# Kernel optimization log

Measured on AMD Instinct MI355X. Metric: run time of the kernel, lower is better.

Reference implementation:

```python
import jax, jax.numpy as jnp
import numpy as np

N_HEAD = 4
GROUPS = 32
EPS = 1e-5


def _group_norm(x, w, b):
    B, C, H, W = x.shape
    g = x.reshape(B, GROUPS, C // GROUPS, H, W)
    mu = g.mean(axis=(2, 3, 4), keepdims=True)
    var = ((g - mu) ** 2).mean(axis=(2, 3, 4), keepdims=True)
    g = (g - mu) * jax.lax.rsqrt(var + EPS)
    return g.reshape(B, C, H, W) * w[None, :, None, None] + b[None, :, None, None]


def _l2norm(x):
    # F.normalize(x, dim=-1): x / max(||x||_2, 1e-12)
    n = jnp.sqrt(jnp.sum(x * x, axis=-1, keepdims=True))
    return x / jnp.maximum(n, 1e-12)


def _masked_softmax(attn, kk):
    # topk indices -> scatter 1s -> masked softmax (faithful to torch scatter_ path)
    idx = jax.lax.top_k(attn, kk)[1]                      # [B,H,c,kk]
    mask = jax.nn.one_hot(idx, attn.shape[-1], dtype=attn.dtype).sum(-2)  # [B,H,c,c]
    return jax.nn.softmax(jnp.where(mask > 0, attn, -jnp.inf), axis=-1)


def setup_inputs() -> dict:
    key = jax.random.key(0)
    ks = jax.random.split(key, 8)
    B, C, H, W = 4, 256, 128, 128
    x = jax.random.normal(ks[0], (B, C, H, W), jnp.float32)
    gn_w = 1.0 + 0.02 * jax.random.normal(ks[1], (C,), jnp.float32)
    gn_b = 0.02 * jax.random.normal(ks[2], (C,), jnp.float32)
    w_qkv = jax.random.normal(ks[3], (3 * C, C), jnp.float32) / np.sqrt(C).astype(np.float32)
    w_dw = jax.random.normal(ks[4], (3 * C, 1, 3, 3), jnp.float32) / 3.0
    w_out = jax.random.normal(ks[5], (C, C), jnp.float32) / np.sqrt(C).astype(np.float32)
    b_out = 0.01 * jax.random.normal(ks[6], (C,), jnp.float32)
    temperature = jnp.ones((N_HEAD, 1, 1), jnp.float32)
    attn_w = jnp.full((4,), 0.2, jnp.float32)  # attn1..attn4 combine weights
    return dict(x=x, gn_w=gn_w, gn_b=gn_b, w_qkv=w_qkv, w_dw=w_dw,
                w_out=w_out, b_out=b_out, temperature=temperature, attn_w=attn_w)


def reference(x, gn_w, gn_b, w_qkv, w_dw, w_out, b_out, temperature, attn_w):
    B, C, H, W = x.shape
    c = C // N_HEAD
    xn = _group_norm(x, gn_w, gn_b)
    # 1x1 conv (no bias)
    qkv = jnp.einsum('oi,bihw->bohw', w_qkv, xn)
    # 3x3 depthwise conv, padding=1, groups=3C, no bias
    qkv = jax.lax.conv_general_dilated(
        qkv, w_dw, window_strides=(1, 1), padding=((1, 1), (1, 1)),
        feature_group_count=3 * C,
        dimension_numbers=('NCHW', 'OIHW', 'NCHW'))
    q, k, v = jnp.split(qkv, 3, axis=1)
    # b (head c) h w -> b head c (h w)
    q = q.reshape(B, N_HEAD, c, H * W)
    k = k.reshape(B, N_HEAD, c, H * W)
    v = v.reshape(B, N_HEAD, c, H * W)
    q = _l2norm(q)
    k = _l2norm(k)
    # FFT cross-correlation attention (fftshift over ALL axes, as torch default)
    q_fft = jnp.fft.fftshift(jnp.fft.rfft2(q))   # [B,H,c,HW//2+1] complex
    k_fft = jnp.fft.fftshift(jnp.fft.rfft2(k))
    attn = jnp.einsum('bhcf,bhdf->bhcd', q_fft, k_fft) * temperature  # complex [B,H,c,c]
    attn = jnp.fft.irfft2(jnp.fft.ifftshift(attn), s=(c, c))          # real [B,H,c,c]
    ks_list = [c // 2, (c * 2) // 3, (c * 3) // 4, (c * 4) // 5]
    out = None
    for i, kk in enumerate(ks_list):
        a = _masked_softmax(attn, kk)
        o = jnp.einsum('bhcd,bhds->bhcs', a, v) * attn_w[i]
        out = o if out is None else out + o
    out = out.reshape(B, C, H, W)
    out = jnp.einsum('oi,bihw->bohw', w_out, out) + b_out[None, :, None, None]
    return out
```

## Files before the change

### kernel.cpp

```cpp
#include <hip/hip_runtime.h>
#include <math.h>

#define NC 256
#define CH3 768
#define HWSZ 16384

typedef __attribute__((ext_vector_type(8))) short short8;
typedef __attribute__((ext_vector_type(4))) float f32x4;
typedef __attribute__((ext_vector_type(4))) unsigned int u32x4;

static const size_t OFF_TW1   = 0;
static const size_t OFF_TW2   = 32768;
static const size_t OFF_HM    = 65536;
static const size_t OFF_SCALE = 65600;
static const size_t OFF_SHIFT = 66624;
static const size_t OFF_PACK  = 67648;
static const size_t OFF_AW    = 182336;
static const size_t OFF_GNP   = 444480;
static const size_t SHARED_END= 446528;

static const size_t R_QKV  = 0;
static const size_t R_SCR  = 12582912;
static const size_t R_H    = 25165824;
static const size_t R_PP   = 29360128;
static const size_t R_RP   = 30408704;
static const size_t R_ATTN = 31457280;
static const size_t R_ACOMB= 31473664;
static const size_t R_PS   = 31490048;
static const size_t R_RS   = 31506432;
static const size_t R_DWP  = 31522816;
static const size_t R_SSUM = 31532032;
static const size_t R_SALT = 31532800;
static const size_t R_SSQ  = 31533568;
static const size_t RSTRIDE= 31534336;
static const size_t HNOFF  = 8388608;

#define TDA_RH 0
#define TDA_RL 8192
#define TDA_IH 16384
#define TDA_IL 24576
#define ETA_RH 32768
#define ETA_RL 40960
#define ETA_IH 49152
#define ETA_IL 57344
#define STB_RH 65536
#define STB_RL 73728
#define STB_IH 81920
#define STB_IL 90112
#define STB_NIH 98304
#define STB_NIL 106496

#define AWQ_H 0
#define AWQ_L 98304
#define AWO_H 196608
#define AWO_L 229376

__device__ inline unsigned short b16rn(float x){
  unsigned u = __float_as_uint(x);
  return (unsigned short)((u + 0x7FFFu + ((u>>16)&1u)) >> 16);
}
__device__ inline unsigned int pk_hi(float x, float y){
  return (__float_as_uint(x)>>16) | (__float_as_uint(y) & 0xFFFF0000u);
}
__device__ inline unsigned int pk_lo(float x, float y){
  float xl = x - __uint_as_float(__float_as_uint(x) & 0xFFFF0000u);
  float yl = y - __uint_as_float(__float_as_uint(y) & 0xFFFF0000u);
  return (unsigned)b16rn(xl) | ((unsigned)b16rn(yl)<<16);
}
__device__ inline short8 ld8g(const unsigned int* p){ return *(const short8*)p; }

__global__ __launch_bounds__(256) void init_tables_k(float* __restrict__ ws){
  int idx = blockIdx.x*256 + threadIdx.x;
  float2* tw1 = (float2*)(ws + OFF_TW1);
  float2* tw2 = (float2*)(ws + OFF_TW2);
  unsigned int* pk = (unsigned int*)(ws + OFF_PACK);
  const double P2 = 6.283185307179586476925286766559005;
  int m = idx >> 7, k = idx & 127;
  double a2 = P2 * (double)(m*k) / 16384.0;
  tw1[idx] = make_float2((float)cos(a2), (float)(-sin(a2)));
  tw2[idx] = make_float2((float)cos(a2), (float)( sin(a2)));
  if (idx < 64){
    double acc = 0.0;
    for (int v = 1; v < 32; v++) acc += sin(P2 * (double)((v*idx) & 63) / 64.0);
    ws[OFF_HM + idx] = (float)(-acc / 32.0);
  }
  if (idx < 8192){
    int r = idx >> 6, kp = idx & 63;
    int k0 = 2*kp, k1 = 2*kp+1;
    double a0 = P2 * (double)((r*k0) & 127) / 128.0;
    double a1 = P2 * (double)((r*k1) & 127) / 128.0;
    float c0 = (float)cos(a0), c1 = (float)cos(a1);
    float s0 = (float)sin(a0), s1 = (float)sin(a1);
    pk[TDA_RH + idx] = pk_hi(c0, c1);  pk[TDA_RL + idx] = pk_lo(c0, c1);
    pk[TDA_IH + idx] = pk_hi(-s0,-s1); pk[TDA_IL + idx] = pk_lo(-s0,-s1);
    pk[ETA_RH + idx] = pk_hi(c0, c1);  pk[ETA_RL + idx] = pk_lo(c0, c1);
    pk[ETA_IH + idx] = pk_hi(s0, s1);  pk[ETA_IL + idx] = pk_lo(s0, s1);
    float sr0, si0, sr1, si1;
    {
      int d0 = (r - k0) & 127, d1 = (r - k1) & 127;
      if (d0 == 0){ sr0 = 64.f; si0 = 0.f; }
      else if ((d0 & 1) == 0){ sr0 = 0.f; si0 = 0.f; }
      else { double th = 3.1415926535897932384626 * (double)d0 / 128.0;
             sr0 = 1.f; si0 = (float)(cos(th)/sin(th)); }
      if (d1 == 0){ sr1 = 64.f; si1 = 0.f; }
      else if ((d1 & 1) == 0){ sr1 = 0.f; si1 = 0.f; }
      else { double th = 3.1415926535897932384626 * (double)d1 / 128.0;
             sr1 = 1.f; si1 = (float)(cos(th)/sin(th)); }
    }
    pk[STB_RH + idx]  = pk_hi(sr0, sr1);  pk[STB_RL + idx]  = pk_lo(sr0, sr1);
    pk[STB_IH + idx]  = pk_hi(si0, si1);  pk[STB_IL + idx]  = pk_lo(si0, si1);
    pk[STB_NIH + idx] = pk_hi(-si0,-si1); pk[STB_NIL + idx] = pk_lo(-si0,-si1);
  }
}

__global__ __launch_bounds__(256) void wpack_k(const float* __restrict__ wqkv, const float* __restrict__ wout,
                                               unsigned int* __restrict__ aw){
  int id = blockIdx.x*256 + threadIdx.x;
  int row = id >> 7, kp = id & 127;
  if (row < CH3){
    float v0 = wqkv[row*256 + 2*kp], v1 = wqkv[row*256 + 2*kp + 1];
    aw[AWQ_H + row*128 + kp] = pk_hi(v0, v1);
    aw[AWQ_L + row*128 + kp] = pk_lo(v0, v1);
  } else {
    int r2 = row - CH3;
    float v0 = wout[r2*256 + 2*kp], v1 = wout[r2*256 + 2*kp + 1];
    aw[AWO_H + r2*128 + kp] = pk_hi(v0, v1);
    aw[AWO_L + r2*128 + kp] = pk_lo(v0, v1);
  }
}

__global__ __launch_bounds__(256) void gn_part_k(const float* __restrict__ x, float2* __restrict__ part){
  int id = blockIdx.x;
  const float4* p = (const float4*)(x + (size_t)id*HWSZ);
  int tid = threadIdx.x;
  float s = 0.f, sq = 0.f;
  #pragma unroll
  for (int i = 0; i < 16; i++){
    float4 v = p[tid + i*256];
    s  += v.x+v.y+v.z+v.w;
    sq += v.x*v.x+v.y*v.y+v.z*v.z+v.w*v.w;
  }
  __shared__ float r1[256], r2[256];
  r1[tid]=s; r2[tid]=sq; __syncthreads();
  for (int off=128; off; off>>=1){
    if (tid<off){ r1[tid]+=r1[tid+off]; r2[tid]+=r2[tid+off]; }
    __syncthreads();
  }
  if (tid==0) part[id] = make_float2(r1[0], r2[0]);
}
__global__ __launch_bounds__(128) void gn_fin_k(const float2* __restrict__ part, const float* __restrict__ gw,
                                                const float* __restrict__ gb, float* __restrict__ scale,
                                                float* __restrict__ shift){
  int bg = threadIdx.x;
  int b = bg >> 5, g = bg & 31;
  float s = 0.f, sq = 0.f;
  #pragma unroll
  for (int i = 0; i < 8; i++){
    float2 v = part[b*NC + g*8 + i];
    s += v.x; sq += v.y;
  }
  const float n = 8.0f*HWSZ;
  float mu = s/n, var = sq/n - mu*mu;
  float rs = rsqrtf(var + 1e-5f);
  for (int i = 0; i < 8; i++){
    int ch = g*8 + i;
    float sc = rs * gw[ch];
    scale[b*NC + ch] = sc;
    shift[b*NC + ch] = gb[ch] - mu*sc;
  }
}

__global__ __launch_bounds__(256) void packx_k(const float* __restrict__ xbase, const float* __restrict__ scale,
                                               const float* __restrict__ shift, float* __restrict__ R0,
                                               size_t rstride){
  int bz = blockIdx.z;
  const float* xb = xbase + (size_t)bz*NC*HWSZ;
  const float* sc = scale + bz*NC;
  const float* sh = shift + bz*NC;
  unsigned int* BqH = (unsigned int*)(R0 + (size_t)bz*rstride + R_H);
  unsigned int* BqL = BqH + 2097152;
  int kb = blockIdx.y;
  int n = blockIdx.x*256 + threadIdx.x;
  float v[8];
  #pragma unroll
  for (int c = 0; c < 8; c++){
    int ch = kb*8 + c;
    v[c] = xb[(size_t)ch*HWSZ + n]*sc[ch] + sh[ch];
  }
  u32x4 h, l;
  #pragma unroll
  for (int q = 0; q < 4; q++){
    h[q] = pk_hi(v[2*q], v[2*q+1]);
    l[q] = pk_lo(v[2*q], v[2*q+1]);
  }
  *(u32x4*)&BqH[((size_t)kb*HWSZ + n)*4] = h;
  *(u32x4*)&BqL[((size_t)kb*HWSZ + n)*4] = l;
}

__global__ __launch_bounds__(256) void gemm_pk(const unsigned int* __restrict__ Ah, const unsigned int* __restrict__ Al,
                                               const unsigned int* __restrict__ Bh0, const unsigned int* __restrict__ Bl0,
                                               const float* __restrict__ bias, float* __restrict__ C0,
                                               size_t bstride, size_t cstride){
  const unsigned int* Bh = Bh0 + (size_t)blockIdx.z*bstride;
  const unsigned int* Bl = Bl0 + (size_t)blockIdx.z*bstride;
  float* C = C0 + (size_t)blockIdx.z*cstride;
  int tid = threadIdx.x;
  int lane = tid & 63, wid = tid >> 6;
  int m0 = blockIdx.y*128, n0 = blockIdx.x*128;
  int wr = (wid>>1)*64, wc = (wid&1)*64;
  int lr = lane & 15, lk = lane >> 4;
  f32x4 acc[4][4] = {};
  size_t aoff[4], boff[4];
  #pragma unroll
  for (int i=0;i<4;i++) aoff[i] = (size_t)(m0 + wr + i*16 + lr)*128 + lk*4;
  #pragma unroll
  for (int j=0;j<4;j++) boff[j] = ((size_t)lk*HWSZ + n0 + wc + j*16 + lr)*4;
  short8 aH[2][4], aL[2][4], bH[2][4], bL[2][4];
  #pragma unroll
  for (int i=0;i<4;i++){ aH[0][i] = ld8g(Ah + aoff[i]); aL[0][i] = ld8g(Al + aoff[i]); }
  #pragma unroll
  for (int j=0;j<4;j++){ bH[0][j] = ld8g(Bh + boff[j]); bL[0][j] = ld8g(Bl + boff[j]); }
  #pragma unroll
  for (int kt = 0; kt < 8; kt++){
    int cur = kt & 1, nxt = cur ^ 1;
    if (kt < 7){
      size_t da = (size_t)(kt+1)*16;
      size_t db = (size_t)(kt+1)*4*HWSZ*4;
      #pragma unroll
      for (int i=0;i<4;i++){ aH[nxt][i] = ld8g(Ah + aoff[i] + da); aL[nxt][i] = ld8g(Al + aoff[i] + da); }
      #pragma unroll
      for (int j=0;j<4;j++){ bH[nxt][j] = ld8g(Bh + boff[j] + db); bL[nxt][j] = ld8g(Bl + boff[j] + db); }
    }
    #pragma unroll
    for (int i=0;i<4;i++)
      #pragma unroll
      for (int j=0;j<4;j++){
        acc[i][j] = __builtin_amdgcn_mfma_f32_16x16x32_bf16(aH[cur][i], bH[cur][j], acc[i][j], 0,0,0);
        acc[i][j] = __builtin_amdgcn_mfma_f32_16x16x32_bf16(aH[cur][i], bL[cur][j], acc[i][j], 0,0,0);
        acc[i][j] = __builtin_amdgcn_mfma_f32_16x16x32_bf16(aL[cur][i], bH[cur][j], acc[i][j], 0,0,0);
      }
  }
  #pragma unroll
  for (int i=0;i<4;i++){
    #pragma unroll
    for (int e=0;e<4;e++){
      int row = m0 + wr + i*16 + lk*4 + e;
      float bb = bias ? bias[row] : 0.0f;
      #pragma unroll
      for (int j=0;j<4;j++)
        C[(size_t)row*HWSZ + n0 + wc + j*16 + lr] = acc[i][j][e] + bb;
    }
  }
}

__global__ __launch_bounds__(256) void dwconv_tiled_k(float* __restrict__ R0, size_t rstride,
                                                      const float* __restrict__ wdw){
  float* Rb = R0 + (size_t)blockIdx.y*rstride;
  int blk = blockIdx.x;
  int ch = blk >> 2, sl = blk & 3;
  int h0 = sl*32;
  const float* in = Rb + R_SCR + (size_t)ch*HWSZ;
  float* part = Rb + R_DWP;
  float w[9];
  #pragma unroll
  for (int i=0;i<9;i++) w[i] = wdw[ch*9+i];
  __shared__ float tile[34][132];
  __shared__ float r0[256], r1[256], r2[256];
  int tid = threadIdx.x;
  #pragma unroll
  for (int i = 0; i < 5; i++){
    int id = tid + i*256;
    if (id < 1088){
      int r = id >> 5, c4 = id & 31;
      int gh = h0 - 1 + r;
      float4 v = (gh >= 0 && gh < 128) ? *(const float4*)&in[gh*128 + c4*4]
                                       : make_float4(0.f,0.f,0.f,0.f);
      *(float4*)&tile[r][c4*4] = v;
    }
  }
  __syncthreads();
  float s=0.f, sa=0.f, sq=0.f;
  #pragma unroll
  for (int it=0; it<4; it++){
    int idx = it*256 + tid;
    int lh = idx >> 5;
    int xq = idx & 31;
    int xb4 = xq*4;
    float o[4];
    #pragma unroll
    for (int e=0;e<4;e++){
      int xw = xb4 + e;
      float acc = 0.f;
      #pragma unroll
      for (int ky=0; ky<3; ky++){
        const float* tr = &tile[lh+ky][xw];
        if (xw > 0)   acc += tr[-1]*w[ky*3+0];
                      acc += tr[ 0]*w[ky*3+1];
        if (xw < 127) acc += tr[ 1]*w[ky*3+2];
      }
      o[e] = acc;
      s += acc; sq += acc*acc;
      sa += (e & 1) ? -acc : acc;
    }
    int sbase = (h0+lh)*128 + xb4;
    if (ch < 256){
      unsigned short* QHo = (unsigned short*)(Rb + R_QKV);
      unsigned short* QLo = (unsigned short*)(Rb + R_QKV + 2097152);
      size_t ro = (size_t)ch*HWSZ;
      #pragma unroll
      for (int e=0;e<4;e++){
        int sf = (16384 - (sbase+e)) & 16383;
        unsigned u = __float_as_uint(o[e]);
        QHo[ro + sf] = (unsigned short)(u >> 16);
        QLo[ro + sf] = b16rn(o[e] - __uint_as_float(u & 0xFFFF0000u));
      }
    } else if (ch < 512){
      *(float4*)&(Rb + R_QKV + (size_t)ch*HWSZ)[sbase] = make_float4(o[0],o[1],o[2],o[3]);
      unsigned short* KHo = (unsigned short*)(Rb + R_H);
      unsigned short* KLo = (unsigned short*)(Rb + R_H + 2097152);
      size_t ro = (size_t)(ch-256)*HWSZ;
      #pragma unroll
      for (int e=0;e<4;e++){
        unsigned u = __float_as_uint(o[e]);
        KHo[ro + sbase+e] = (unsigned short)(u >> 16);
        KLo[ro + sbase+e] = b16rn(o[e] - __uint_as_float(u & 0xFFFF0000u));
      }
    } else {
      *(float4*)&(Rb + R_QKV + (size_t)ch*HWSZ)[sbase] = make_float4(o[0],o[1],o[2],o[3]);
    }
  }
  r0[tid]=s; r1[tid]=sa; r2[tid]=sq; __syncthreads();
  for (int off=128; off; off>>=1){
    if (tid<off){ r0[tid]+=r0[tid+off]; r1[tid]+=r1[tid+off]; r2[tid]+=r2[tid+off]; }
    __syncthreads();
  }
  if (tid==0){ part[blk]=r0[0]; part[3072+blk]=r1[0]; part[6144+blk]=r2[0]; }
}

__global__ __launch_bounds__(256) void fft1_mfma_k(const float* __restrict__ ws, float* __restrict__ R0,
                                                   size_t rstride){
  float* Rb = R0 + (size_t)blockIdx.y*rstride;
  const float* Kb = Rb + R_QKV + (size_t)256*HWSZ;
  float2* Tc = (float2*)(Rb + R_SCR);
  const unsigned int* PK = (const unsigned int*)(ws + OFF_PACK);
  const float2* tw1 = (const float2*)(ws + OFF_TW1);
  __shared__ unsigned int Bth[128][20], Btl[128][20];
  int tid = threadIdx.x;
  int lane = tid & 63, wid = tid >> 6;
  int wr = (wid>>1)*64, wc = (wid&1)*64;
  int lr = lane & 15, lk = lane >> 4;
  int row = blockIdx.x;
  const float* src = Kb + (size_t)row*HWSZ;
  f32x4 aR[4][4] = {}, aI[4][4] = {};
  int bc = tid & 127, grp = tid >> 7;
  for (int kt = 0; kt < 4; kt++){
    #pragma unroll
    for (int p=0;p<8;p++){
      int kp = grp*8 + p;
      int a = kt*32 + 2*kp;
      float v0 = src[a*128 + bc], v1 = src[(a+1)*128 + bc];
      Bth[bc][kp] = pk_hi(v0, v1);
      Btl[bc][kp] = pk_lo(v0, v1);
    }
    __syncthreads();
    short8 bh[4], bl[4];
    #pragma unroll
    for (int j=0;j<4;j++){
      bh[j] = *(const short8*)&Bth[wc + j*16 + lr][lk*4];
      bl[j] = *(const short8*)&Btl[wc + j*16 + lr][lk*4];
    }
    #pragma unroll
    for (int i=0;i<4;i++){
      int off = (wr + i*16 + lr)*64 + kt*16 + lk*4;
      short8 ahR = ld8g(PK + TDA_RH + off), alR = ld8g(PK + TDA_RL + off);
      short8 ahI = ld8g(PK + TDA_IH + off), alI = ld8g(PK + TDA_IL + off);
      #pragma unroll
      for (int j=0;j<4;j++){
        aR[i][j] = __builtin_amdgcn_mfma_f32_16x16x32_bf16(ahR, bh[j], aR[i][j], 0,0,0);
        aR[i][j] = __builtin_amdgcn_mfma_f32_16x16x32_bf16(ahR, bl[j], aR[i][j], 0,0,0);
        aR[i][j] = __builtin_amdgcn_mfma_f32_16x16x32_bf16(alR, bh[j], aR[i][j], 0,0,0);
        aI[i][j] = __builtin_amdgcn_mfma_f32_16x16x32_bf16(ahI, bh[j], aI[i][j], 0,0,0);
        aI[i][j] = __builtin_amdgcn_mfma_f32_16x16x32_bf16(ahI, bl[j], aI[i][j], 0,0,0);
        aI[i][j] = __builtin_amdgcn_mfma_f32_16x16x32_bf16(alI, bh[j], aI[i][j], 0,0,0);
      }
    }
    __syncthreads();
  }
  #pragma unroll
  for (int i=0;i<4;i++)
    #pragma unroll
    for (int e=0;e<4;e++){
      int m = wr + i*16 + lk*4 + e;
      #pragma unroll
      for (int j=0;j<4;j++){
        int col = wc + j*16 + lr;
        float2 t = tw1[m*128 + col];
        float r = aR[i][j][e], im = aI[i][j][e];
        Tc[(size_t)m*32768 + row*128 + col] = make_float2(r*t.x - im*t.y, r*t.y + im*t.x);
      }
    }
}

__global__ __launch_bounds__(256) void fft2_mfma_k(const float* __restrict__ ws, float* __restrict__ R0,
                                                   size_t rstride){
  float* Rb = R0 + (size_t)blockIdx.y*rstride;
  float2* TU = (float2*)(Rb + R_SCR);
  const unsigned int* PK = (const unsigned int*)(ws + OFF_PACK);
  const float2* tw2 = (const float2*)(ws + OFF_TW2);
  __shared__ unsigned int ARh[128][20], ARl[128][20], AIh[128][20], AIl[128][20];
  int tid = threadIdx.x;
  int lane = tid & 63, wid = tid >> 6;
  int wr = (wid>>1)*64, wc = (wid&1)*64;
  int lr = lane & 15, lk = lane >> 4;
  int m0 = blockIdx.x*128;
  f32x4 aR[4][4] = {}, aI[4][4] = {};
  const float* Tf = (const float*)TU;
  for (int kt = 0; kt < 4; kt++){
    #pragma unroll
    for (int s=0;s<8;s++){
      int id = tid + s*256;
      int r = id >> 4, kp = id & 15;
      int k = kt*32 + 2*kp;
      float4 v = *(const float4*)&Tf[((size_t)(m0+r)*128 + k)*2];
      ARh[r][kp] = pk_hi(v.x, v.z); ARl[r][kp] = pk_lo(v.x, v.z);
      AIh[r][kp] = pk_hi(v.y, v.w); AIl[r][kp] = pk_lo(v.y, v.w);
    }
    __syncthreads();
    short8 ahR[4], alR[4], ahI[4], alI[4];
    #pragma unroll
    for (int i=0;i<4;i++){
      int ar = wr + i*16 + lr;
      ahR[i] = *(const short8*)&ARh[ar][lk*4];
      alR[i] = *(const short8*)&ARl[ar][lk*4];
      ahI[i] = *(const short8*)&AIh[ar][lk*4];
      alI[i] = *(const short8*)&AIl[ar][lk*4];
    }
    #pragma unroll
    for (int j=0;j<4;j++){
      int boff = (wc + j*16 + lr)*64 + kt*16 + lk*4;
      short8 bhR = ld8g(PK + STB_RH + boff), blR = ld8g(PK + STB_RL + boff);
      short8 bhI = ld8g(PK + STB_IH + boff), blI = ld8g(PK + STB_IL + boff);
      short8 bhN = ld8g(PK + STB_NIH + boff), blN = ld8g(PK + STB_NIL + boff);
      #pragma unroll
      for (int i=0;i<4;i++){
        aR[i][j] = __builtin_amdgcn_mfma_f32_16x16x32_bf16(ahR[i], bhR, aR[i][j], 0,0,0);
        aR[i][j] = __builtin_amdgcn_mfma_f32_16x16x32_bf16(ahR[i], blR, aR[i][j], 0,0,0);
        aR[i][j] = __builtin_amdgcn_mfma_f32_16x16x32_bf16(alR[i], bhR, aR[i][j], 0,0,0);
        aR[i][j] = __builtin_amdgcn_mfma_f32_16x16x32_bf16(ahI[i], bhN, aR[i][j], 0,0,0);
        aR[i][j] = __builtin_amdgcn_mfma_f32_16x16x32_bf16(ahI[i], blN, aR[i][j], 0,0,0);
        aR[i][j] = __builtin_amdgcn_mfma_f32_16x16x32_bf16(alI[i], bhN, aR[i][j], 0,0,0);
        aI[i][j] = __builtin_amdgcn_mfma_f32_16x16x32_bf16(ahR[i], bhI, aI[i][j], 0,0,0);
        aI[i][j] = __builtin_amdgcn_mfma_f32_16x16x32_bf16(ahR[i], blI, aI[i][j], 0,0,0);
        aI[i][j] = __builtin_amdgcn_mfma_f32_16x16x32_bf16(alR[i], bhI, aI[i][j], 0,0,0);
        aI[i][j] = __builtin_amdgcn_mfma_f32_16x16x32_bf16(ahI[i], bhR, aI[i][j], 0,0,0);
        aI[i][j] = __builtin_amdgcn_mfma_f32_16x16x32_bf16(ahI[i], blR, aI[i][j], 0,0,0);
        aI[i][j] = __builtin_amdgcn_mfma_f32_16x16x32_bf16(alI[i], bhR, aI[i][j], 0,0,0);
      }
    }
    __syncthreads();
  }
  #pragma unroll
  for (int i=0;i<4;i++)
    #pragma unroll
    for (int e=0;e<4;e++){
      int m = m0 + wr + i*16 + lk*4 + e;
      int f0 = m >> 8;
      #pragma unroll
      for (int j=0;j<4;j++){
        int col = wc + j*16 + lr;
        float2 t = tw2[f0*128 + col];
        float r = aR[i][j][e], im = aI[i][j][e];
        TU[(size_t)m*128 + col] = make_float2(r*t.x - im*t.y, r*t.y + im*t.x);
      }
    }
}

__global__ __launch_bounds__(256) void fft3_mfma_k(const float* __restrict__ ws, float* __restrict__ R0,
                                                   size_t rstride){
  float* Rb = R0 + (size_t)blockIdx.y*rstride;
  const float2* U = (const float2*)(Rb + R_SCR);
  unsigned short* HHo = (unsigned short*)(Rb + R_SCR + HNOFF);
  unsigned short* HLo = (unsigned short*)(Rb + R_SCR + HNOFF + 2097152);
  const unsigned int* PK = (const unsigned int*)(ws + OFF_PACK);
  __shared__ unsigned int BRh[128][20], BRl[128][20], BIh[128][20], BIl[128][20];
  int tid = threadIdx.x;
  int lane = tid & 63, wid = tid >> 6;
  int wr = (wid>>1)*64, wc = (wid&1)*64;
  int lr = lane & 15, lk = lane >> 4;
  int brow = blockIdx.x;
  f32x4 ac[4][4] = {};
  int bc = tid & 127, grp = tid >> 7;
  for (int kt = 0; kt < 4; kt++){
    #pragma unroll
    for (int p=0;p<8;p++){
      int kp = grp*8 + p;
      int k = kt*32 + 2*kp;
      float2 v0 = U[((size_t)k*256 + brow)*128 + bc];
      float2 v1 = U[((size_t)(k+1)*256 + brow)*128 + bc];
      BRh[bc][kp] = pk_hi(v0.x, v1.x); BRl[bc][kp] = pk_lo(v0.x, v1.x);
      BIh[bc][kp] = pk_hi(v0.y, v1.y); BIl[bc][kp] = pk_lo(v0.y, v1.y);
    }
    __syncthreads();
    short8 ahR[4], alR[4], ahI[4], alI[4];
    #pragma unroll
    for (int i=0;i<4;i++){
      int off = (wr + i*16 + lr)*64 + kt*16 + lk*4;
      ahR[i] = ld8g(PK + ETA_RH + off); alR[i] = ld8g(PK + ETA_RL + off);
      ahI[i] = ld8g(PK + ETA_IH + off); alI[i] = ld8g(PK + ETA_IL + off);
    }
    #pragma unroll
    for (int j=0;j<4;j++){
      int col = wc + j*16 + lr;
      short8 bhR = *(const short8*)&BRh[col][lk*4];
      short8 blR = *(const short8*)&BRl[col][lk*4];
      short8 bhI = *(const short8*)&BIh[col][lk*4];
      short8 blI = *(const short8*)&BIl[col][lk*4];
      #pragma unroll
      for (int i=0;i<4;i++){
        ac[i][j] = __builtin_amdgcn_mfma_f32_16x16x32_bf16(ahR[i], bhI, ac[i][j], 0,0,0);
        ac[i][j] = __builtin_amdgcn_mfma_f32_16x16x32_bf16(ahR[i], blI, ac[i][j], 0,0,0);
        ac[i][j] = __builtin_amdgcn_mfma_f32_16x16x32_bf16(alR[i], bhI, ac[i][j], 0,0,0);
        ac[i][j] = __builtin_amdgcn_mfma_f32_16x16x32_bf16(ahI[i], bhR, ac[i][j], 0,0,0);
        ac[i][j] = __builtin_amdgcn_mfma_f32_16x16x32_bf16(ahI[i], blR, ac[i][j], 0,0,0);
        ac[i][j] = __builtin_amdgcn_mfma_f32_16x16x32_bf16(alI[i], bhR, ac[i][j], 0,0,0);
      }
    }
    __syncthreads();
  }
  #pragma unroll
  for (int i=0;i<4;i++)
    #pragma unroll
    for (int e=0;e<4;e++){
      int m = wr + i*16 + lk*4 + e;
      #pragma unroll
      for (int j=0;j<4;j++){
        int col = wc + j*16 + lr;
        float v = ac[i][j][e];
        unsigned u = __float_as_uint(v);
        size_t o = (size_t)brow*HWSZ + m*128 + col;
        HHo[o] = (unsigned short)(u >> 16);
        HLo[o] = b16rn(v - __uint_as_float(u & 0xFFFF0000u));
      }
    }
}

__global__ __launch_bounds__(256) void pri3_k(float* __restrict__ R0, size_t rstride){
  float* Rb = R0 + (size_t)blockIdx.z*rstride;
  int sp = blockIdx.x, head = blockIdx.y;
  const unsigned short* QH = (const unsigned short*)(Rb + R_QKV);
  const unsigned short* QL = (const unsigned short*)(Rb + R_QKV + 2097152);
  const unsigned short* KH = (const unsigned short*)(Rb + R_H);
  const unsigned short* KL = (const unsigned short*)(Rb + R_H + 2097152);
  const unsigned short* HH = (const unsigned short*)(Rb + R_SCR + HNOFF);
  const unsigned short* HL = (const unsigned short*)(Rb + R_SCR + HNOFF + 2097152);
  float* Pp = Rb + R_PP;
  float* Rp = Rb + R_RP;
  int tid = threadIdx.x, lane = tid & 63, wid = tid >> 6;
  int wr = (wid>>1)*32, wc = (wid&1)*32;
  int lr = lane & 15, lk = lane >> 4;
  size_t qoff[2], koff[2];
  #pragma unroll
  for (int i=0;i<2;i++) qoff[i] = (size_t)(head*64 + wr + i*16 + lr)*HWSZ + sp*256 + lk*8;
  #pragma unroll
  for (int j=0;j<2;j++) koff[j] = (size_t)(head*64 + wc + j*16 + lr)*HWSZ + sp*256 + lk*8;
  f32x4 aP[2][2] = {}, aRi[2][2] = {};
  short8 qh[2][2], ql[2][2], k1h[2][2], k1l[2][2], k2h[2][2], k2l[2][2];
#define LDPRI(B,T) { int d = (T)*32; \
    _Pragma("unroll") \
    for (int i=0;i<2;i++){ \
      qh[B][i] = *(const short8*)(QH + qoff[i] + d); \
      ql[B][i] = *(const short8*)(QL + qoff[i] + d); } \
    _Pragma("unroll") \
    for (int j=0;j<2;j++){ \
      k1h[B][j] = *(const short8*)(KH + koff[j] + d); \
      k1l[B][j] = *(const short8*)(KL + koff[j] + d); \
      k2h[B][j] = *(const short8*)(HH + koff[j] + d); \
      k2l[B][j] = *(const short8*)(HL + koff[j] + d); } }
  LDPRI(0,0);
  #pragma unroll
  for (int kt = 0; kt < 8; kt++){
    int cur = kt & 1;
    if (kt < 7) LDPRI(cur^1, kt+1);
    #pragma unroll
    for (int i=0;i<2;i++)
      #pragma unroll
      for (int j=0;j<2;j++){
        aP[i][j]  = __builtin_amdgcn_mfma_f32_16x16x32_bf16(qh[cur][i], k1h[cur][j], aP[i][j], 0,0,0);
        aP[i][j]  = __builtin_amdgcn_mfma_f32_16x16x32_bf16(qh[cur][i], k1l[cur][j], aP[i][j], 0,0,0);
        aP[i][j]  = __builtin_amdgcn_mfma_f32_16x16x32_bf16(ql[cur][i], k1h[cur][j], aP[i][j], 0,0,0);
        aRi[i][j] = __builtin_amdgcn_mfma_f32_16x16x32_bf16(qh[cur][i], k2h[cur][j], aRi[i][j], 0,0,0);
        aRi[i][j] = __builtin_amdgcn_mfma_f32_16x16x32_bf16(qh[cur][i], k2l[cur][j], aRi[i][j], 0,0,0);
        aRi[i][j] = __builtin_amdgcn_mfma_f32_16x16x32_bf16(ql[cur][i], k2h[cur][j], aRi[i][j], 0,0,0);
      }
  }
#undef LDPRI
  size_t obase = ((size_t)(sp*4 + head)) << 12;
  #pragma unroll
  for (int i=0;i<2;i++)
    #pragma unroll
    for (int e=0;e<4;e++){
      int row = wr + i*16 + lk*4 + e;
      #pragma unroll
      for (int j=0;j<2;j++){
        int col = wc + j*16 + lr;
        size_t o = obase + (size_t)row*64 + col;
        Pp[o] = aP[i][j][e];
        Rp[o] = aRi[i][j][e];
      }
    }
}

__global__ __launch_bounds__(256) void red_k(float* __restrict__ R0, size_t rstride){
  float* Rb = R0 + (size_t)blockIdx.y*rstride;
  const float* Pp = Rb + R_PP;
  const float* Rp = Rb + R_RP;
  float* Ps = Rb + R_PS;
  float* Rs = Rb + R_RS;
  int tid = threadIdx.x;
  #pragma unroll
  for (int rep=0; rep<2; rep++){
    int g = blockIdx.x*512 + rep*256 + tid;
    int head = g >> 12, loc = g & 4095;
    float p = 0.f, ri = 0.f;
    for (int sp=0; sp<64; sp++){
      size_t o = ((size_t)(sp*4+head)<<12) + loc;
      p += Pp[o]; ri += Rp[o];
    }
    Ps[g] = p; Rs[g] = ri;
  }
  if (blockIdx.x == 0){
    const float* part = Rb + R_DWP;
    for (int ch = tid; ch < CH3; ch += 256){
      float s=0.f, sa=0.f, sq=0.f;
      #pragma unroll
      for (int sl=0; sl<4; sl++){
        s  += part[ch*4+sl];
        sa += part[3072+ch*4+sl];
        sq += part[6144+ch*4+sl];
      }
      Rb[R_SSUM+ch]=s; Rb[R_SALT+ch]=sa; Rb[R_SSQ+ch]=sq;
    }
  }
}

__global__ __launch_bounds__(256) void attn_build_k(const float* __restrict__ ws, float* __restrict__ R0,
                                                    size_t rstride, const float* __restrict__ temperature){
  float* Rb = R0 + (size_t)blockIdx.y*rstride;
  const float* Ps   = Rb + R_PS;
  const float* Rs   = Rb + R_RS;
  const float* ssum = Rb + R_SSUM;
  const float* salt = Rb + R_SALT;
  const float* ssq  = Rb + R_SSQ;
  float* attn = Rb + R_ATTN;
  const float* hmg  = ws + OFF_HM;
  __shared__ float Rn[64][65], Ril[64][65], hm[64];
  int head = blockIdx.x;
  int tid = threadIdx.x;
  if (tid < 64) hm[tid] = hmg[tid];
  for (int t=0;t<16;t++){
    int idx = tid + t*256; int c = idx>>6, d = idx&63;
    float P = Ps[head*4096 + idx], Ri = Rs[head*4096 + idx];
    int qch = head*64 + c;
    int kch = 256 + head*64 + d;
    float qs=ssum[qch], qa=salt[qch], qn=fmaxf(sqrtf(ssq[qch]), 1e-12f);
    float ks=ssum[kch], ka=salt[kch], kn=fmaxf(sqrtf(ssq[kch]), 1e-12f);
    float Rr = 0.5f*(16384.0f*P + qs*ks + qa*ka);
    float sc = 1.0f/(qn*kn);
    Rn[c][d]  = Rr*sc;
    Ril[c][d] = Ri*sc;
  }
  __syncthreads();
  float tmp2 = temperature[(head+2)&3];
  for (int t=0;t<16;t++){
    int idx = tid + t*256; int c = idx>>6, e = idx&63;
    float s = Rn[c][e];
    #pragma unroll 8
    for (int d=0; d<64; d++) s += Ril[c][d]*hm[(e-d)&63];
    attn[((size_t)head<<12) + (size_t)(c*64+e)] = s*tmp2;
  }
}

__global__ __launch_bounds__(64) void topk_k(float* __restrict__ R0, size_t rstride,
                                             const float* __restrict__ attn_w){
  float* Rb = R0 + (size_t)blockIdx.y*rstride;
  const float* attn = Rb + R_ATTN;
  float* Acomb = Rb + R_ACOMB;
  int blk = blockIdx.x;
  int tid = threadIdx.x;
  __shared__ float row[64];
  float v = attn[(size_t)blk*64 + tid];
  row[tid] = v;
  __syncthreads();
  int rank = 0; float vmax = -1e30f;
  for (int l=0;l<64;l++){
    float w = row[l];
    if (w > v || (w == v && l < tid)) rank++;
    vmax = fmaxf(vmax, w);
  }
  float e = expf(v - vmax);
  const int kks[4] = {32,42,48,51};
  float denom[4];
  #pragma unroll
  for (int i=0;i<4;i++){
    float x = (rank < kks[i]) ? e : 0.0f;
    #pragma unroll
    for (int off=32; off; off>>=1) x += __shfl_xor(x, off);
    denom[i] = x;
  }
  float wgt = 0.f;
  #pragma unroll
  for (int i=0;i<4;i++) if (rank < kks[i]) wgt += attn_w[i] / denom[i];
  Acomb[(size_t)blk*64 + tid] = e * wgt;
}

__global__ __launch_bounds__(256) void av_k(float* __restrict__ R0, size_t rstride){
  float* Rb = R0 + (size_t)blockIdx.z*rstride;
  const float* Acomb = Rb + R_ACOMB;
  unsigned int* BqH = (unsigned int*)(Rb + R_H);
  unsigned int* BqL = BqH + 2097152;
  int head = blockIdx.y;
  int n0 = blockIdx.x*64;
  const float* Vb = Rb + R_QKV + (size_t)(512 + head*64)*HWSZ;
  __shared__ float As[64][65], Bs[16][65];
  int tid=threadIdx.x, tx=tid&15, ty=tid>>4;
  for (int t=0;t<16;t++){ int idx=tid+t*256; As[idx>>6][idx&63] = Acomb[((size_t)head<<12)+idx]; }
  __syncthreads();
  float acc[4][4]={};
  for (int k0=0;k0<64;k0+=16){
    #pragma unroll
    for (int i=0;i<4;i++){ int id=tid+i*256; int nn=id&63, k=id>>6;
      Bs[k][nn] = Vb[(size_t)(k0+k)*HWSZ + n0+nn]; }
    __syncthreads();
    #pragma unroll
    for (int k=0;k<16;k++){
      float a[4], bv[4];
      #pragma unroll
      for (int i=0;i<4;i++) a[i]=As[ty*4+i][k0+k];
      #pragma unroll
      for (int j=0;j<4;j++) bv[j]=Bs[k][tx*4+j];
      #pragma unroll
      for (int i=0;i<4;i++)
        #pragma unroll
        for (int j=0;j<4;j++) acc[i][j] += a[i]*bv[j];
    }
    __syncthreads();
  }
  int kpa = head*32 + ty*2;
  int kba = kpa >> 2, qa = kpa & 3;
  int kpb = kpa + 1;
  int kbb = kpb >> 2, qb = kpb & 3;
  #pragma unroll
  for (int j=0;j<4;j++){
    int n = n0 + tx*4 + j;
    BqH[((size_t)kba*HWSZ + n)*4 + qa] = pk_hi(acc[0][j], acc[1][j]);
    BqL[((size_t)kba*HWSZ + n)*4 + qa] = pk_lo(acc[0][j], acc[1][j]);
    BqH[((size_t)kbb*HWSZ + n)*4 + qb] = pk_hi(acc[2][j], acc[3][j]);
    BqL[((size_t)kbb*HWSZ + n)*4 + qb] = pk_lo(acc[2][j], acc[3][j]);
  }
}

extern "C" void kernel_launch(void* const* d_in, const int* in_sizes, int n_in,
                              void* d_out, int out_size, void* d_ws, size_t ws_size,
                              hipStream_t stream) {
  const float* x     = (const float*)d_in[0];
  const float* gn_w  = (const float*)d_in[1];
  const float* gn_b  = (const float*)d_in[2];
  const float* w_qkv = (const float*)d_in[3];
  const float* w_dw  = (const float*)d_in[4];
  const float* w_out = (const float*)d_in[5];
  const float* b_out = (const float*)d_in[6];
  const float* temperature = (const float*)d_in[7];
  const float* attn_w = (const float*)d_in[8];
  float* out = (float*)d_out;
  float* ws  = (float*)d_ws;
  unsigned int* AW = (unsigned int*)(ws + OFF_AW);
  float* R0 = ws + SHARED_END;
  const size_t CHW = (size_t)NC*HWSZ;

  size_t need2 = (SHARED_END + 2*RSTRIDE)*sizeof(float);
  size_t need4 = (SHARED_END + 4*RSTRIDE)*sizeof(float);
  int zb = (ws_size >= need4) ? 4 : (ws_size >= need2) ? 2 : 1;

  init_tables_k<<<64,256,0,stream>>>(ws);
  wpack_k<<<512,256,0,stream>>>(w_qkv, w_out, AW);
  gn_part_k<<<1024,256,0,stream>>>(x, (float2*)(ws+OFF_GNP));
  gn_fin_k<<<1,128,0,stream>>>((const float2*)(ws+OFF_GNP), gn_w, gn_b,
                               ws+OFF_SCALE, ws+OFF_SHIFT);

  for (int b0 = 0; b0 < 4; b0 += zb){
    packx_k<<<dim3(64,32,zb),256,0,stream>>>(x + (size_t)b0*CHW, ws+OFF_SCALE+b0*NC,
                                             ws+OFF_SHIFT+b0*NC, R0, RSTRIDE);
    gemm_pk<<<dim3(128,6,zb),256,0,stream>>>(AW+AWQ_H, AW+AWQ_L,
                                             (unsigned int*)(R0+R_H), (unsigned int*)(R0+R_H)+2097152,
                                             nullptr, R0+R_SCR, RSTRIDE, RSTRIDE);
    dwconv_tiled_k<<<dim3(3072,zb),256,0,stream>>>(R0, RSTRIDE, w_dw);
    fft1_mfma_k<<<dim3(256,zb),256,0,stream>>>(ws, R0, RSTRIDE);
    fft2_mfma_k<<<dim3(256,zb),256,0,stream>>>(ws, R0, RSTRIDE);
    fft3_mfma_k<<<dim3(256,zb),256,0,stream>>>(ws, R0, RSTRIDE);
    pri3_k<<<dim3(64,4,zb),256,0,stream>>>(R0, RSTRIDE);
    red_k<<<dim3(32,zb),256,0,stream>>>(R0, RSTRIDE);
    attn_build_k<<<dim3(4,zb),256,0,stream>>>(ws, R0, RSTRIDE, temperature);
    topk_k<<<dim3(256,zb),64,0,stream>>>(R0, RSTRIDE, attn_w);
    av_k<<<dim3(256,4,zb),256,0,stream>>>(R0, RSTRIDE);
    gemm_pk<<<dim3(128,2,zb),256,0,stream>>>(AW+AWO_H, AW+AWO_L,
                                             (unsigned int*)(R0+R_H), (unsigned int*)(R0+R_H)+2097152,
                                             b_out, out + (size_t)b0*CHW, RSTRIDE, CHW);
  }
}
```

Baseline: 825.1 us.

## Store FFT intermediates as pre-split bf16 hi/lo planes, drop LDS staging

The FFT stage kernels now write intermediates as separate bf16 high/low planes in layouts the next stage can load directly as MFMA fragments, instead of fp32 complex buffers that were re-split through shared memory. fft1 reads the K planes already produced by dwconv, so the fp32 K copy is no longer stored. fft2 and fft3 drop their LDS staging and barriers, and fft2 is split into 512 smaller blocks. This cuts conversion work and intermediate memory traffic, but the direct global fragment loads and the new strided layouts may coalesce less well.

Result: slower. 906.5 us (+9.9%).

```diff
diff --git a/kernel.cpp b/kernel.cpp
--- a/kernel.cpp
+++ b/kernel.cpp
@@ -33,7 +33,8 @@
 static const size_t R_SALT = 31532800;
 static const size_t R_SSQ  = 31533568;
 static const size_t RSTRIDE= 31534336;
-static const size_t HNOFF  = 8388608;
+static const size_t UROFF  = 4194304;
+static const size_t UIOFF  = 8388608;
 
 #define TDA_RH 0
 #define TDA_RL 8192
@@ -68,6 +69,12 @@
   return (unsigned)b16rn(xl) | ((unsigned)b16rn(yl)<<16);
 }
 __device__ inline short8 ld8g(const unsigned int* p){ return *(const short8*)p; }
+__device__ inline short8 ld8s(const unsigned short* p){ return *(const short8*)p; }
+__device__ inline void wr_split(unsigned short* H, unsigned short* L, size_t o, float v){
+  unsigned u = __float_as_uint(v);
+  H[o] = (unsigned short)(u >> 16);
+  L[o] = b16rn(v - __uint_as_float(u & 0xFFFF0000u));
+}
 
 __global__ __launch_bounds__(256) void init_tables_k(float* __restrict__ ws){
   int idx = blockIdx.x*256 + threadIdx.x;
@@ -310,21 +317,15 @@
       #pragma unroll
       for (int e=0;e<4;e++){
         int sf = (16384 - (sbase+e)) & 16383;
-        unsigned u = __float_as_uint(o[e]);
-        QHo[ro + sf] = (unsigned short)(u >> 16);
-        QLo[ro + sf] = b16rn(o[e] - __uint_as_float(u & 0xFFFF0000u));
+        wr_split(QHo, QLo, ro + sf, o[e]);
       }
     } else if (ch < 512){
-      *(float4*)&(Rb + R_QKV + (size_t)ch*HWSZ)[sbase] = make_float4(o[0],o[1],o[2],o[3]);
       unsigned short* KHo = (unsigned short*)(Rb + R_H);
       unsigned short* KLo = (unsigned short*)(Rb + R_H + 2097152);
       size_t ro = (size_t)(ch-256)*HWSZ;
       #pragma unroll
-      for (int e=0;e<4;e++){
-        unsigned u = __float_as_uint(o[e]);
-        KHo[ro + sbase+e] = (unsigned short)(u >> 16);
-        KLo[ro + sbase+e] = b16rn(o[e] - __uint_as_float(u & 0xFFFF0000u));
-      }
+      for (int e=0;e<4;e++)
+        wr_split(KHo, KLo, ro + sbase+e, o[e]);
     } else {
       *(float4*)&(Rb + R_QKV + (size_t)ch*HWSZ)[sbase] = make_float4(o[0],o[1],o[2],o[3]);
     }
@@ -340,8 +341,12 @@
 __global__ __launch_bounds__(256) void fft1_mfma_k(const float* __restrict__ ws, float* __restrict__ R0,
                                                    size_t rstride){
   float* Rb = R0 + (size_t)blockIdx.y*rstride;
-  const float* Kb = Rb + R_QKV + (size_t)256*HWSZ;
-  float2* Tc = (float2*)(Rb + R_SCR);
+  const unsigned short* KH = (const unsigned short*)(Rb + R_H);
+  const unsigned short* KL = (const unsigned short*)(Rb + R_H + 2097152);
+  unsigned short* TRH = (unsigned short*)(Rb + R_SCR);
+  unsigned short* TRL = TRH + 4194304;
+  unsigned short* TIH = TRL + 4194304;
+  unsigned short* TIL = TIH + 4194304;
   const unsigned int* PK = (const unsigned int*)(ws + OFF_PACK);
   const float2* tw1 = (const float2*)(ws + OFF_TW1);
   __shared__ unsigned int Bth[128][20], Btl[128][20];
@@ -350,7 +355,6 @@
   int wr = (wid>>1)*64, wc = (wid&1)*64;
   int lr = lane & 15, lk = lane >> 4;
   int row = blockIdx.x;
-  const float* src = Kb + (size_t)row*HWSZ;
   f32x4 aR[4][4] = {}, aI[4][4] = {};
   int bc = tid & 127, grp = tid >> 7;
   for (int kt = 0; kt < 4; kt++){
@@ -358,9 +362,9 @@
     for (int p=0;p<8;p++){
       int kp = grp*8 + p;
       int a = kt*32 + 2*kp;
-      float v0 = src[a*128 + bc], v1 = src[(a+1)*128 + bc];
-      Bth[bc][kp] = pk_hi(v0, v1);
-      Btl[bc][kp] = pk_lo(v0, v1);
+      size_t o0 = (size_t)row*HWSZ + a*128 + bc;
+      Bth[bc][kp] = (unsigned)KH[o0] | ((unsigned)KH[o0+128] << 16);
+      Btl[bc][kp] = (unsigned)KL[o0] | ((unsigned)KL[o0+128] << 16);
     }
     __syncthreads();
     short8 bh[4], bl[4];
@@ -396,7 +400,10 @@
         int col = wc + j*16 + lr;
         float2 t = tw1[m*128 + col];
         float r = aR[i][j][e], im = aI[i][j][e];
-        Tc[(size_t)m*32768 + row*128 + col] = make_float2(r*t.x - im*t.y, r*t.y + im*t.x);
+        float vr = r*t.x - im*t.y, vi = r*t.y + im*t.x;
+        size_t o = (size_t)m*32768 + row*128 + col;
+        wr_split(TRH, TRL, o, vr);
+        wr_split(TIH, TIL, o, vi);
       }
     }
 }
@@ -404,36 +411,32 @@
 __global__ __launch_bounds__(256) void fft2_mfma_k(const float* __restrict__ ws, float* __restrict__ R0,
                                                    size_t rstride){
   float* Rb = R0 + (size_t)blockIdx.y*rstride;
-  float2* TU = (float2*)(Rb + R_SCR);
+  const unsigned short* TRH = (const unsigned short*)(Rb + R_SCR);
+  const unsigned short* TRL = TRH + 4194304;
+  const unsigned short* TIH = TRL + 4194304;
+  const unsigned short* TIL = TIH + 4194304;
+  unsigned short* URH = (unsigned short*)(Rb + R_QKV + UROFF);
+  unsigned short* URL = URH + 4194304;
+  unsigned short* UIH = (unsigned short*)(Rb + R_SCR + UIOFF);
+  unsigned short* UIL = UIH + 4194304;
   const unsigned int* PK = (const unsigned int*)(ws + OFF_PACK);
   const float2* tw2 = (const float2*)(ws + OFF_TW2);
-  __shared__ unsigned int ARh[128][20], ARl[128][20], AIh[128][20], AIl[128][20];
-  int tid = threadIdx.x;
-  int lane = tid & 63, wid = tid >> 6;
-  int wr = (wid>>1)*64, wc = (wid&1)*64;
+  int tid = threadIdx.x, lane = tid & 63, wid = tid >> 6;
+  int row = blockIdx.x >> 1, mh = blockIdx.x & 1;
+  int wr = (wid>>1)*32, wc = (wid&1)*64;
   int lr = lane & 15, lk = lane >> 4;
-  int m0 = blockIdx.x*128;
-  f32x4 aR[4][4] = {}, aI[4][4] = {};
-  const float* Tf = (const float*)TU;
+  f32x4 aR[2][4] = {}, aI[2][4] = {};
+  size_t aoff[2];
+  #pragma unroll
+  for (int i=0;i<2;i++) aoff[i] = (size_t)(mh*64 + wr + i*16 + lr)*32768 + row*128 + lk*8;
+  #pragma unroll
   for (int kt = 0; kt < 4; kt++){
-    #pragma unroll
-    for (int s=0;s<8;s++){
-      int id = tid + s*256;
-      int r = id >> 4, kp = id & 15;
-      int k = kt*32 + 2*kp;
-      float4 v = *(const float4*)&Tf[((size_t)(m0+r)*128 + k)*2];
-      ARh[r][kp] = pk_hi(v.x, v.z); ARl[r][kp] = pk_lo(v.x, v.z);
-      AIh[r][kp] = pk_hi(v.y, v.w); AIl[r][kp] = pk_lo(v.y, v.w);
-    }
-    __syncthreads();
-    short8 ahR[4], alR[4], ahI[4], alI[4];
-    #pragma unroll
-    for (int i=0;i<4;i++){
-      int ar = wr + i*16 + lr;
-      ahR[i] = *(const short8*)&ARh[ar][lk*4];
-      alR[i] = *(const short8*)&ARl[ar][lk*4];
-      ahI[i] = *(const short8*)&AIh[ar][lk*4];
-      alI[i] = *(const short8*)&AIl[ar][lk*4];
+    short8 ahR[2], alR[2], ahI[2], alI[2];
+    #pragma unroll
+    for (int i=0;i<2;i++){
+      size_t o = aoff[i] + kt*32;
+      ahR[i] = ld8s(TRH + o); alR[i] = ld8s(TRL + o);
+      ahI[i] = ld8s(TIH + o); alI[i] = ld8s(TIL + o);
     }
     #pragma unroll
     for (int j=0;j<4;j++){
@@ -442,7 +445,7 @@
       short8 bhI = ld8g(PK + STB_IH + boff), blI = ld8g(PK + STB_IL + boff);
       short8 bhN = ld8g(PK + STB_NIH + boff), blN = ld8g(PK + STB_NIL + boff);
       #pragma unroll
-      for (int i=0;i<4;i++){
+      for (int i=0;i<2;i++){
         aR[i][j] = __builtin_amdgcn_mfma_f32_16x16x32_bf16(ahR[i], bhR, aR[i][j], 0,0,0);
         aR[i][j] = __builtin_amdgcn_mfma_f32_16x16x32_bf16(ahR[i], blR, aR[i][j], 0,0,0);
         aR[i][j] = __builtin_amdgcn_mfma_f32_16x16x32_bf16(alR[i], bhR, aR[i][j], 0,0,0);
@@ -457,75 +460,77 @@
         aI[i][j] = __builtin_amdgcn_mfma_f32_16x16x32_bf16(alI[i], bhR, aI[i][j], 0,0,0);
       }
     }
-    __syncthreads();
-  }
-  #pragma unroll
-  for (int i=0;i<4;i++)
-    #pragma unroll
-    for (int e=0;e<4;e++){
-      int m = m0 + wr + i*16 + lk*4 + e;
-      int f0 = m >> 8;
-      #pragma unroll
-      for (int j=0;j<4;j++){
-        int col = wc + j*16 + lr;
-        float2 t = tw2[f0*128 + col];
-        float r = aR[i][j][e], im = aI[i][j][e];
-        TU[(size_t)m*128 + col] = make_float2(r*t.x - im*t.y, r*t.y + im*t.x);
-      }
-    }
+  }
+  #pragma unroll
+  for (int i=0;i<2;i++){
+    int f0b = mh*64 + wr + i*16 + lk*4;
+    #pragma unroll
+    for (int j=0;j<4;j++){
+      int r = wc + j*16 + lr;
+      unsigned long long prH=0ull, prL=0ull, piH=0ull, piL=0ull;
+      #pragma unroll
+      for (int e=0;e<4;e++){
+        float2 t = tw2[(f0b+e)*128 + r];
+        float rr = aR[i][j][e], ii = aI[i][j][e];
+        float ur = rr*t.x - ii*t.y, ui = rr*t.y + ii*t.x;
+        unsigned uur = __float_as_uint(ur), uui = __float_as_uint(ui);
+        prH |= (unsigned long long)(uur >> 16) << (16*e);
+        prL |= (unsigned long long)b16rn(ur - __uint_as_float(uur & 0xFFFF0000u)) << (16*e);
+        piH |= (unsigned long long)(uui >> 16) << (16*e);
+        piL |= (unsigned long long)b16rn(ui - __uint_as_float(uui & 0xFFFF0000u)) << (16*e);
+      }
+      size_t o = (size_t)row*HWSZ + r*128 + f0b;
+      *(unsigned long long*)(URH + o) = prH;
+      *(unsigned long long*)(URL + o) = prL;
+      *(unsigned long long*)(UIH + o) = piH;
+      *(unsigned long long*)(UIL + o) = piL;
+    }
+  }
 }
 
 __global__ __launch_bounds__(256) void fft3_mfma_k(const float* __restrict__ ws, float* __restrict__ R0,
                                                    size_t rstride){
   float* Rb = R0 + (size_t)blockIdx.y*rstride;
-  const float2* U = (const float2*)(Rb + R_SCR);
-  unsigned short* HHo = (unsigned short*)(Rb + R_SCR + HNOFF);
-  unsigned short* HLo = (unsigned short*)(Rb + R_SCR + HNOFF + 2097152);
+  const unsigned short* URH = (const unsigned short*)(Rb + R_QKV + UROFF);
+  const unsigned short* URL = URH + 4194304;
+  const unsigned short* UIH = (const unsigned short*)(Rb + R_SCR + UIOFF);
+  const unsigned short* UIL = UIH + 4194304;
+  unsigned short* HNH = (unsigned short*)(Rb + R_SCR);
+  unsigned short* HNL = HNH + 4194304;
   const unsigned int* PK = (const unsigned int*)(ws + OFF_PACK);
-  __shared__ unsigned int BRh[128][20], BRl[128][20], BIh[128][20], BIl[128][20];
-  int tid = threadIdx.x;
-  int lane = tid & 63, wid = tid >> 6;
+  int tid = threadIdx.x, lane = tid & 63, wid = tid >> 6;
   int wr = (wid>>1)*64, wc = (wid&1)*64;
   int lr = lane & 15, lk = lane >> 4;
-  int brow = blockIdx.x;
+  int row = blockIdx.x;
   f32x4 ac[4][4] = {};
-  int bc = tid & 127, grp = tid >> 7;
+  size_t boff[4];
+  #pragma unroll
+  for (int j=0;j<4;j++) boff[j] = (size_t)row*HWSZ + (wc + j*16 + lr)*128 + lk*8;
+  #pragma unroll
   for (int kt = 0; kt < 4; kt++){
-    #pragma unroll
-    for (int p=0;p<8;p++){
-      int kp = grp*8 + p;
-      int k = kt*32 + 2*kp;
-      float2 v0 = U[((size_t)k*256 + brow)*128 + bc];
-      float2 v1 = U[((size_t)(k+1)*256 + brow)*128 + bc];
-      BRh[bc][kp] = pk_hi(v0.x, v1.x); BRl[bc][kp] = pk_lo(v0.x, v1.x);
-      BIh[bc][kp] = pk_hi(v0.y, v1.y); BIl[bc][kp] = pk_lo(v0.y, v1.y);
-    }
-    __syncthreads();
-    short8 ahR[4], alR[4], ahI[4], alI[4];
+    short8 bRh[4], bRl[4], bIh[4], bIl[4];
+    #pragma unroll
+    for (int j=0;j<4;j++){
+      bRh[j] = ld8s(URH + boff[j] + kt*32);
+      bRl[j] = ld8s(URL + boff[j] + kt*32);
+      bIh[j] = ld8s(UIH + boff[j] + kt*32);
+      bIl[j] = ld8s(UIL + boff[j] + kt*32);
+    }
     #pragma unroll
     for (int i=0;i<4;i++){
       int off = (wr + i*16 + lr)*64 + kt*16 + lk*4;
-      ahR[i] = ld8g(PK + ETA_RH + off); alR[i] = ld8g(PK + ETA_RL + off);
-      ahI[i] = ld8g(PK + ETA_IH + off); alI[i] = ld8g(PK + ETA_IL + off);
-    }
-    #pragma unroll
-    for (int j=0;j<4;j++){
-      int col = wc + j*16 + lr;
-      short8 bhR = *(const short8*)&BRh[col][lk*4];
-      short8 blR = *(const short8*)&BRl[col][lk*4];
-      short8 bhI = *(const short8*)&BIh[col][lk*4];
-      short8 blI = *(const short8*)&BIl[col][lk*4];
-      #pragma unroll
-      for (int i=0;i<4;i++){
-        ac[i][j] = __builtin_amdgcn_mfma_f32_16x16x32_bf16(ahR[i], bhI, ac[i][j], 0,0,0);
-        ac[i][j] = __builtin_amdgcn_mfma_f32_16x16x32_bf16(ahR[i], blI, ac[i][j], 0,0,0);
-        ac[i][j] = __builtin_amdgcn_mfma_f32_16x16x32_bf16(alR[i], bhI, ac[i][j], 0,0,0);
-        ac[i][j] = __builtin_amdgcn_mfma_f32_16x16x32_bf16(ahI[i], bhR, ac[i][j], 0,0,0);
-        ac[i][j] = __builtin_amdgcn_mfma_f32_16x16x32_bf16(ahI[i], blR, ac[i][j], 0,0,0);
-        ac[i][j] = __builtin_amdgcn_mfma_f32_16x16x32_bf16(alI[i], bhR, ac[i][j], 0,0,0);
-      }
-    }
-    __syncthreads();
+      short8 ahR = ld8g(PK + ETA_RH + off), alR = ld8g(PK + ETA_RL + off);
+      short8 ahI = ld8g(PK + ETA_IH + off), alI = ld8g(PK + ETA_IL + off);
+      #pragma unroll
+      for (int j=0;j<4;j++){
+        ac[i][j] = __builtin_amdgcn_mfma_f32_16x16x32_bf16(ahR, bIh[j], ac[i][j], 0,0,0);
+        ac[i][j] = __builtin_amdgcn_mfma_f32_16x16x32_bf16(ahR, bIl[j], ac[i][j], 0,0,0);
+        ac[i][j] = __builtin_amdgcn_mfma_f32_16x16x32_bf16(alR, bIh[j], ac[i][j], 0,0,0);
+        ac[i][j] = __builtin_amdgcn_mfma_f32_16x16x32_bf16(ahI, bRh[j], ac[i][j], 0,0,0);
+        ac[i][j] = __builtin_amdgcn_mfma_f32_16x16x32_bf16(ahI, bRl[j], ac[i][j], 0,0,0);
+        ac[i][j] = __builtin_amdgcn_mfma_f32_16x16x32_bf16(alI, bRh[j], ac[i][j], 0,0,0);
+      }
+    }
   }
   #pragma unroll
   for (int i=0;i<4;i++)
@@ -535,11 +540,7 @@
       #pragma unroll
       for (int j=0;j<4;j++){
         int col = wc + j*16 + lr;
-        float v = ac[i][j][e];
-        unsigned u = __float_as_uint(v);
-        size_t o = (size_t)brow*HWSZ + m*128 + col;
-        HHo[o] = (unsigned short)(u >> 16);
-        HLo[o] = b16rn(v - __uint_as_float(u & 0xFFFF0000u));
+        wr_split(HNH, HNL, (size_t)row*HWSZ + m*128 + col, ac[i][j][e]);
       }
     }
 }
@@ -551,8 +552,8 @@
   const unsigned short* QL = (const unsigned short*)(Rb + R_QKV + 2097152);
   const unsigned short* KH = (const unsigned short*)(Rb + R_H);
   const unsigned short* KL = (const unsigned short*)(Rb + R_H + 2097152);
-  const unsigned short* HH = (const unsigned short*)(Rb + R_SCR + HNOFF);
-  const unsigned short* HL = (const unsigned short*)(Rb + R_SCR + HNOFF + 2097152);
+  const unsigned short* HNH = (const unsigned short*)(Rb + R_SCR);
+  const unsigned short* HNL = HNH + 4194304;
   float* Pp = Rb + R_PP;
   float* Rp = Rb + R_RP;
   int tid = threadIdx.x, lane = tid & 63, wid = tid >> 6;
@@ -568,14 +569,14 @@
 #define LDPRI(B,T) { int d = (T)*32; \
     _Pragma("unroll") \
     for (int i=0;i<2;i++){ \
-      qh[B][i] = *(const short8*)(QH + qoff[i] + d); \
-      ql[B][i] = *(const short8*)(QL + qoff[i] + d); } \
+      qh[B][i] = ld8s(QH + qoff[i] + d); \
+      ql[B][i] = ld8s(QL + qoff[i] + d); } \
     _Pragma("unroll") \
     for (int j=0;j<2;j++){ \
-      k1h[B][j] = *(const short8*)(KH + koff[j] + d); \
-      k1l[B][j] = *(const short8*)(KL + koff[j] + d); \
-      k2h[B][j] = *(const short8*)(HH + koff[j] + d); \
-      k2l[B][j] = *(const short8*)(HL + koff[j] + d); } }
+      k1h[B][j] = ld8s(KH + koff[j] + d); \
+      k1l[B][j] = ld8s(KL + koff[j] + d); \
+      k2h[B][j] = ld8s(HNH + koff[j] + d); \
+      k2l[B][j] = ld8s(HNL + koff[j] + d); } }
   LDPRI(0,0);
   #pragma unroll
   for (int kt = 0; kt < 8; kt++){
@@ -795,7 +796,7 @@
                                              nullptr, R0+R_SCR, RSTRIDE, RSTRIDE);
     dwconv_tiled_k<<<dim3(3072,zb),256,0,stream>>>(R0, RSTRIDE, w_dw);
     fft1_mfma_k<<<dim3(256,zb),256,0,stream>>>(ws, R0, RSTRIDE);
-    fft2_mfma_k<<<dim3(256,zb),256,0,stream>>>(ws, R0, RSTRIDE);
+    fft2_mfma_k<<<dim3(512,zb),256,0,stream>>>(ws, R0, RSTRIDE);
     fft3_mfma_k<<<dim3(256,zb),256,0,stream>>>(ws, R0, RSTRIDE);
     pri3_k<<<dim3(64,4,zb),256,0,stream>>>(R0, RSTRIDE);
     red_k<<<dim3(32,zb),256,0,stream>>>(R0, RSTRIDE);
```
